# Performance work log

Measured on AMD Instinct MI355X. Metric: run time of the kernel, lower is better.

The kernel has to match this reference:

```python
import jax, jax.numpy as jnp
import numpy as np

B, S, H, D = 4, 2048, 16, 64
DM = H * D  # d_model = 1024


def setup_inputs() -> dict:
    key = jax.random.key(0)
    ks = jax.random.split(key, 11)
    s = 1.0 / np.sqrt(DM)
    return {
        "query": jax.random.normal(ks[0], (B, S, DM), jnp.float32),
        "key": jax.random.normal(ks[1], (B, S, DM), jnp.float32),
        "value": jax.random.normal(ks[2], (B, S, DM), jnp.float32),
        "Wq": jax.random.uniform(ks[3], (DM, DM), jnp.float32, -s, s),
        "bq": jax.random.uniform(ks[4], (DM,), jnp.float32, -s, s),
        "Wk": jax.random.uniform(ks[5], (DM, DM), jnp.float32, -s, s),
        "bk": jax.random.uniform(ks[6], (DM,), jnp.float32, -s, s),
        "Wv": jax.random.uniform(ks[7], (DM, DM), jnp.float32, -s, s),
        "bv": jax.random.uniform(ks[8], (DM,), jnp.float32, -s, s),
        "Wo": jax.random.uniform(ks[9], (DM, DM), jnp.float32, -s, s),
        "bo": jax.random.uniform(ks[10], (DM,), jnp.float32, -s, s),
        "masking": 1,
    }


def reference(query, key, value, Wq, bq, Wk, bk, Wv, bv, Wo, bo, masking):
    b, s, _ = query.shape
    # Linear projections (torch Linear: x @ W.T + b), split into heads
    q = (query @ Wq.T + bq).reshape(b, s, H, D).transpose(0, 2, 1, 3)  # [B,H,S,D]
    k = (key @ Wk.T + bk).reshape(b, -1, H, D).transpose(0, 2, 1, 3)
    v = (value @ Wv.T + bv).reshape(b, -1, H, D).transpose(0, 2, 1, 3)
    scores = jnp.einsum("bhqd,bhkd->bhqk", q, k) / np.power(D, 0.5)
    if masking:
        # subsequent (strictly upper-triangular) mask -> fill with -1e9
        sub = jnp.triu(jnp.ones((s, k.shape[2]), bool), k=1)
        scores = jnp.where(sub, jnp.float32(-1e9), scores)
    attn = jax.nn.softmax(scores, axis=-1)
    out = jnp.einsum("bhqk,bhkd->bhqd", attn, v)  # [B,H,S,D]
    out = out.transpose(0, 2, 1, 3).reshape(b, s, H * D)
    return out @ Wo.T + bo
```

## Files before the change

kernel.cpp:

```cpp
#include <hip/hip_runtime.h>
#include <stdint.h>
#include <stddef.h>

#define B_ 4
#define S_ 2048
#define H_ 16
#define D_ 64
#define DM 1024
#define MTOT 8192
#define QSCALE 0.1803368867f

typedef __bf16 bf16x8 __attribute__((ext_vector_type(8)));
typedef __bf16 bf16x4 __attribute__((ext_vector_type(4)));
typedef float  f32x4  __attribute__((ext_vector_type(4)));

__device__ __forceinline__ void g2l16(const void* g, void* l) {
  __builtin_amdgcn_global_load_lds(
      (__attribute__((address_space(1))) void*)g,
      (__attribute__((address_space(3))) void*)l, 16, 0, 0);
}

struct Cvt7 {
  const float* s[7];
  __bf16* d[7];
  float sc[7];
};
__global__ __launch_bounds__(256) void cvt_all(Cvt7 a) {
  const int b = blockIdx.x;
  int seg, i;
  if (b < 24576) { seg = b >> 13; i = ((b & 8191) << 8) + threadIdx.x; }
  else { const int sb = b - 24576; seg = 3 + (sb >> 10); i = ((sb & 1023) << 8) + threadIdx.x; }
  const float sc = a.sc[seg];
  const float4 v = ((const float4*)a.s[seg])[i];
  bf16x4 o;
  o.x = (__bf16)(v.x * sc); o.y = (__bf16)(v.y * sc);
  o.z = (__bf16)(v.z * sc); o.w = (__bf16)(v.w * sc);
  ((bf16x4*)a.d[seg])[i] = o;
}

__device__ __forceinline__ void gemm_main(const __bf16* __restrict__ A,
                                          const __bf16* __restrict__ W,
                                          int m0, int n0,
                                          __bf16* ldsA, __bf16* ldsB,
                                          f32x4 (&acc)[4][4]) {
  const int tid = threadIdx.x;
  const int lane = tid & 63, wave = tid >> 6;
  const int lq = lane & 15, lhi = lane >> 4;
  const int wr = wave >> 1, wc = wave & 1;

  const int srow = tid >> 2;
  const int cso = ((tid & 3) ^ ((srow >> 1) & 3)) * 8;
  const __bf16* pA = A + (size_t)(m0 + srow) * DM + cso;
  const __bf16* pB = W + (size_t)(n0 + srow) * DM + cso;
  const int tid8 = tid * 8;

  const int sx = (lhi ^ ((lq >> 1) & 3)) * 8;
  const int aB = (wr * 64 + lq) * 32 + sx;
  const int bB = (wc * 64 + lq) * 32 + sx;

#define SA(q, ko, bs) g2l16(pA + (size_t)(q) * 64 * DM + (ko), ldsA + (bs) * 4096 + (q) * 2048 + tid8)
#define SB(q, ko, bs) g2l16(pB + (size_t)(q) * 64 * DM + (ko), ldsB + (bs) * 4096 + (q) * 2048 + tid8)

  SA(0, 0, 0); SA(1, 0, 0); SB(0, 0, 0); SB(1, 0, 0);
  SA(0, 32, 1); SA(1, 32, 1); SB(0, 32, 1); SB(1, 32, 1);
  asm volatile("s_waitcnt vmcnt(4)" ::: "memory");
  __builtin_amdgcn_s_barrier();
  __builtin_amdgcn_sched_barrier(0);

  int bR = 0, bN = 1, bS = 2;
  int koS = 64;
#pragma unroll 1
  for (int t = 0; t < 32; ++t) {
    const __bf16* lA = ldsA + bR * 4096;
    const __bf16* lB = ldsB + bR * 4096;
    const bool s2 = t < 30;
    bf16x8 af[4], bf[4];

#pragma unroll
    for (int i = 0; i < 4; ++i) af[i] = *(const bf16x8*)(lA + aB + i * 512);
#pragma unroll
    for (int j = 0; j < 2; ++j) bf[j] = *(const bf16x8*)(lB + bB + j * 512);
    if (s2) { SA(0, koS, bS); SA(1, koS, bS); }
    __builtin_amdgcn_s_barrier();
    __builtin_amdgcn_sched_barrier(0);
    __builtin_amdgcn_s_setprio(1);
#pragma unroll
    for (int i = 0; i < 4; ++i)
#pragma unroll
      for (int j = 0; j < 2; ++j)
        acc[i][j] = __builtin_amdgcn_mfma_f32_16x16x32_bf16(af[i], bf[j], acc[i][j], 0, 0, 0);
    __builtin_amdgcn_s_setprio(0);

#pragma unroll
    for (int j = 2; j < 4; ++j) bf[j] = *(const bf16x8*)(lB + bB + j * 512);
    if (s2) { SB(0, koS, bS); SB(1, koS, bS); }
    if (t < 30) {
      asm volatile("s_waitcnt vmcnt(4)" ::: "memory");
    } else if (t == 30) {
      asm volatile("s_waitcnt vmcnt(0)" ::: "memory");
    }
    __builtin_amdgcn_s_barrier();
    __builtin_amdgcn_sched_barrier(0);
    __builtin_amdgcn_s_setprio(1);
#pragma unroll
    for (int i = 0; i < 4; ++i)
#pragma unroll
      for (int j = 2; j < 4; ++j)
        acc[i][j] = __builtin_amdgcn_mfma_f32_16x16x32_bf16(af[i], bf[j], acc[i][j], 0, 0, 0);
    __builtin_amdgcn_s_setprio(0);

    const int x = bR; bR = bN; bN = bS; bS = x;
    koS += 32;
  }
#undef SA
#undef SB
}

struct QKVArgs {
  const __bf16 *A0, *A1, *A2;
  const __bf16 *W0, *W1, *W2;
  const float *b0, *b1, *b2;
  __bf16 *oQ, *oK, *oVt;
};

__global__ __launch_bounds__(256, 3) void gemm_qkv(QKVArgs args) {
  const int z = blockIdx.z;
  const __bf16* A    = (z == 0) ? args.A0 : (z == 1) ? args.A1 : args.A2;
  const __bf16* W    = (z == 0) ? args.W0 : (z == 1) ? args.W1 : args.W2;
  const float*  bias = (z == 0) ? args.b0 : (z == 1) ? args.b1 : args.b2;
  const float   bsc  = (z == 0) ? QSCALE : 1.0f;

  __shared__ __bf16 ldsA[3 * 4096];
  __shared__ __bf16 ldsB[3 * 4096];

  const int m0 = blockIdx.x * 128;
  const int n0 = blockIdx.y * 128;

  f32x4 acc[4][4] = {};
  gemm_main(A, W, m0, n0, ldsA, ldsB, acc);

  const int lane = threadIdx.x & 63, wave = threadIdx.x >> 6;
  const int lq = lane & 15, lhi = lane >> 4;
  const int wr = wave >> 1, wc = wave & 1;

  if (z < 2) {
    __bf16* out = (z == 0) ? args.oQ : args.oK;
#pragma unroll
    for (int i = 0; i < 4; ++i)
#pragma unroll
      for (int j = 0; j < 4; ++j)
#pragma unroll
        for (int r = 0; r < 4; ++r) {
          const int row = m0 + wr * 64 + i * 16 + lhi * 4 + r;
          const int col = n0 + wc * 64 + j * 16 + lq;
          out[(size_t)row * DM + col] = (__bf16)(acc[i][j][r] + bias[col] * bsc);
        }
  } else {
    __bf16* out = args.oVt;
#pragma unroll
    for (int i = 0; i < 4; ++i)
#pragma unroll
      for (int j = 0; j < 4; ++j)
#pragma unroll
        for (int r = 0; r < 4; ++r) {
          const int row = m0 + wr * 64 + i * 16 + lhi * 4 + r;
          const int col = n0 + wc * 64 + j * 16 + lq;
          const int bb = row >> 11, s = row & 2047;
          const int hh = col >> 6,  d = col & 63;
          out[(((size_t)(bb * H_ + hh) * D_ + d) << 11) + s] =
              (__bf16)(acc[i][j][r] + bias[col]);
        }
  }
}

__global__ __launch_bounds__(256, 3) void gemm_oproj(const __bf16* __restrict__ A,
                                                     const __bf16* __restrict__ W,
                                                     const float* __restrict__ bias,
                                                     float* __restrict__ out) {
  __shared__ __bf16 ldsA[3 * 4096];
  __shared__ __bf16 ldsB[3 * 4096];

  const int m0 = blockIdx.x * 128;
  const int n0 = blockIdx.y * 128;

  f32x4 acc[4][4] = {};
  gemm_main(A, W, m0, n0, ldsA, ldsB, acc);

  const int lane = threadIdx.x & 63, wave = threadIdx.x >> 6;
  const int lq = lane & 15, lhi = lane >> 4;
  const int wr = wave >> 1, wc = wave & 1;

#pragma unroll
  for (int i = 0; i < 4; ++i)
#pragma unroll
    for (int j = 0; j < 4; ++j)
#pragma unroll
      for (int r = 0; r < 4; ++r) {
        const int row = m0 + wr * 64 + i * 16 + lhi * 4 + r;
        const int col = n0 + wc * 64 + j * 16 + lq;
        out[(size_t)row * DM + col] = acc[i][j][r] + bias[col];
      }
}

__global__ __launch_bounds__(256, 3) void attn_kernel(const __bf16* __restrict__ Q,
                                                      const __bf16* __restrict__ K,
                                                      const __bf16* __restrict__ Vt,
                                                      __bf16* __restrict__ O) {
  const int id = blockIdx.x;
  const int slot = id >> 8;
  const int tau = id & 255;
  const int k4 = (tau >> 3) & 3;
  const int bh = ((tau >> 5) << 3) | (tau & 7);
  const int b = bh >> 4, h = bh & 15;

  int tiles[2];
  int ntile;
  if (slot == 0)      { ntile = 1; tiles[0] = 15 - k4; tiles[1] = 0; }
  else if (slot == 1) { ntile = 1; tiles[0] = 8 + k4;  tiles[1] = 0; }
  else                { ntile = 2; tiles[0] = k4;      tiles[1] = 7 - k4; }

  const int wave = threadIdx.x >> 6;
  const int lane = threadIdx.x & 63;
  const int lq = lane & 15, lhi = lane >> 4;

  const __bf16* Qb = Q + (size_t)b * S_ * DM + h * D_;
  const __bf16* Kb = K + (size_t)b * S_ * DM + h * D_;
  const __bf16* Vb = Vt + (size_t)bh * D_ * S_;

  __shared__ __bf16 Ks[2][64 * 64];
  __shared__ __bf16 Vs[2][64 * 64];
  __shared__ __bf16 Ps[4][32 * 72];
  __bf16* const Pw = Ps[wave];

  const int rl = lane >> 3;
  const int cg8 = ((lane & 7) ^ rl) * 8;

  bf16x8 onesb;
#pragma unroll
  for (int q = 0; q < 8; ++q) onesb[q] = (__bf16)1.0f;

  for (int ti = 0; ti < ntile; ++ti) {
    const int t = tiles[ti];
    const int qw0 = t * 128 + wave * 32;
    const int jend = t * 128 + 64;

    if (ti) __syncthreads();

    bf16x8 qb[2][2];
#pragma unroll
    for (int m = 0; m < 2; ++m)
#pragma unroll
      for (int kd = 0; kd < 2; ++kd)
        qb[m][kd] = *(const bf16x8*)(Qb + (size_t)(qw0 + m * 16 + lq) * DM + kd * 32 + lhi * 8);

    f32x4 o_acc[2][4] = {};
    f32x4 o_sum[2] = {};

#pragma unroll
    for (int i = 0; i < 2; ++i) {
      const int row = wave * 16 + i * 8 + rl;
      g2l16(Kb + (size_t)row * DM + cg8, Ks[0] + ((wave * 16 + i * 8) << 6) + lane * 8);
      g2l16(Vb + (size_t)row * S_ + cg8, Vs[0] + ((wave * 16 + i * 8) << 6) + lane * 8);
    }

    int p = 0;
    for (int j0 = 0; j0 <= jend; j0 += 64) {
      __syncthreads();
      if (j0 < jend) {
        const int jn = j0 + 64;
#pragma unroll
        for (int i = 0; i < 2; ++i) {
          const int row = wave * 16 + i * 8 + rl;
          g2l16(Kb + (size_t)(jn + row) * DM + cg8, Ks[p ^ 1] + ((wave * 16 + i * 8) << 6) + lane * 8);
          g2l16(Vb + (size_t)row * S_ + jn + cg8, Vs[p ^ 1] + ((wave * 16 + i * 8) << 6) + lane * 8);
        }
      }

      if (j0 <= qw0 + 31) {
        bf16x8 kf[4][2];
#pragma unroll
        for (int kt = 0; kt < 4; ++kt) {
          const int r = kt * 16 + lq;
#pragma unroll
          for (int kd = 0; kd < 2; ++kd)
            kf[kt][kd] = *(const bf16x8*)(Ks[p] + (r << 6) + (((kd * 4 + lhi) ^ (r & 7)) << 3));
        }

        bf16x8 vf[4][2];
#pragma unroll
        for (int dt = 0; dt < 4; ++dt) {
          const int r = dt * 16 + lq;
#pragma unroll
          for (int kk = 0; kk < 2; ++kk)
            vf[dt][kk] = *(const bf16x8*)(Vs[p] + (r << 6) + (((kk * 4 + lhi) ^ (r & 7)) << 3));
        }

        f32x4 sc[2][4];
        __builtin_amdgcn_s_setprio(1);
#pragma unroll
        for (int m = 0; m < 2; ++m)
#pragma unroll
          for (int kt = 0; kt < 4; ++kt) {
            f32x4 s = {};
            s = __builtin_amdgcn_mfma_f32_16x16x32_bf16(kf[kt][0], qb[m][0], s, 0, 0, 0);
            s = __builtin_amdgcn_mfma_f32_16x16x32_bf16(kf[kt][1], qb[m][1], s, 0, 0, 0);
            sc[m][kt] = s;
          }
        __builtin_amdgcn_s_setprio(0);

#pragma unroll
        for (int m = 0; m < 2; ++m) {
          const bool dg = (j0 + 63 > qw0 + m * 16);
          if (dg) {
            const int thr = qw0 + m * 16 + lq - j0;
#pragma unroll
            for (int kt = 0; kt < 4; ++kt) {
              bf16x4 pk;
#pragma unroll
              for (int r = 0; r < 4; ++r) {
                float v = sc[m][kt][r];
                if (kt * 16 + lhi * 4 + r > thr) v = -1e9f;
                pk[r] = (__bf16)exp2f(v);
              }
              *(bf16x4*)(Pw + (m * 16 + lq) * 72 + kt * 16 + lhi * 4) = pk;
            }
          } else {
#pragma unroll
            for (int kt = 0; kt < 4; ++kt) {
              bf16x4 pk;
#pragma unroll
              for (int r = 0; r < 4; ++r) pk[r] = (__bf16)exp2f(sc[m][kt][r]);
              *(bf16x4*)(Pw + (m * 16 + lq) * 72 + kt * 16 + lhi * 4) = pk;
            }
          }
        }

#pragma unroll
        for (int m = 0; m < 2; ++m) {
          bf16x8 pa[2];
#pragma unroll
          for (int kk = 0; kk < 2; ++kk)
            pa[kk] = *(const bf16x8*)(Pw + (m * 16 + lq) * 72 + kk * 32 + lhi * 8);
          __builtin_amdgcn_s_setprio(1);
          o_sum[m] = __builtin_amdgcn_mfma_f32_16x16x32_bf16(pa[0], onesb, o_sum[m], 0, 0, 0);
          o_sum[m] = __builtin_amdgcn_mfma_f32_16x16x32_bf16(pa[1], onesb, o_sum[m], 0, 0, 0);
#pragma unroll
          for (int dt = 0; dt < 4; ++dt) {
            o_acc[m][dt] = __builtin_amdgcn_mfma_f32_16x16x32_bf16(pa[0], vf[dt][0], o_acc[m][dt], 0, 0, 0);
            o_acc[m][dt] = __builtin_amdgcn_mfma_f32_16x16x32_bf16(pa[1], vf[dt][1], o_acc[m][dt], 0, 0, 0);
          }
          __builtin_amdgcn_s_setprio(0);
        }
      }
      p ^= 1;
    }

#pragma unroll
    for (int m = 0; m < 2; ++m)
#pragma unroll
      for (int r = 0; r < 4; ++r) {
        const float inv = 1.0f / o_sum[m][r];
        const int qrow = qw0 + m * 16 + lhi * 4 + r;
        __bf16* orow = O + ((size_t)b * S_ + qrow) * DM + h * D_;
#pragma unroll
        for (int dt = 0; dt < 4; ++dt)
          orow[dt * 16 + lq] = (__bf16)(o_acc[m][dt][r] * inv);
      }
  }
}

extern "C" void kernel_launch(void* const* d_in, const int* in_sizes, int n_in,
                              void* d_out, int out_size, void* d_ws, size_t ws_size,
                              hipStream_t stream) {
  (void)in_sizes; (void)n_in; (void)out_size; (void)ws_size;
  const float* query = (const float*)d_in[0];
  const float* key   = (const float*)d_in[1];
  const float* value = (const float*)d_in[2];
  const float* Wq = (const float*)d_in[3];
  const float* bq = (const float*)d_in[4];
  const float* Wk = (const float*)d_in[5];
  const float* bk = (const float*)d_in[6];
  const float* Wv = (const float*)d_in[7];
  const float* bv = (const float*)d_in[8];
  const float* Wo = (const float*)d_in[9];
  const float* bo = (const float*)d_in[10];

  const size_t NX = (size_t)MTOT * DM;
  const size_t NW = (size_t)DM * DM;
  __bf16* p = (__bf16*)d_ws;
  __bf16 *Xq = p, *Xk = Xq + NX, *Xv = Xk + NX;
  __bf16 *Wqb = Xv + NX, *Wkb = Wqb + NW, *Wvb = Wkb + NW, *Wob = Wvb + NW;
  __bf16 *Qrm = Wob + NW, *Krm = Qrm + NX, *Vt = Krm + NX, *Orm = Vt + NX;

  Cvt7 ca;
  ca.s[0] = query; ca.s[1] = key; ca.s[2] = value;
  ca.s[3] = Wq; ca.s[4] = Wk; ca.s[5] = Wv; ca.s[6] = Wo;
  ca.d[0] = Xq; ca.d[1] = Xk; ca.d[2] = Xv;
  ca.d[3] = Wqb; ca.d[4] = Wkb; ca.d[5] = Wvb; ca.d[6] = Wob;
  ca.sc[0] = 1.0f; ca.sc[1] = 1.0f; ca.sc[2] = 1.0f;
  ca.sc[3] = QSCALE;
  ca.sc[4] = 1.0f; ca.sc[5] = 1.0f; ca.sc[6] = 1.0f;
  cvt_all<<<28672, 256, 0, stream>>>(ca);

  QKVArgs qa;
  qa.A0 = Xq; qa.A1 = Xk; qa.A2 = Xv;
  qa.W0 = Wqb; qa.W1 = Wkb; qa.W2 = Wvb;
  qa.b0 = bq; qa.b1 = bk; qa.b2 = bv;
  qa.oQ = Qrm; qa.oK = Krm; qa.oVt = Vt;
  gemm_qkv<<<dim3(MTOT / 128, DM / 128, 3), 256, 0, stream>>>(qa);

  attn_kernel<<<dim3(768), 256, 0, stream>>>(Qrm, Krm, Vt, Orm);

  gemm_oproj<<<dim3(MTOT / 128, DM / 128), 256, 0, stream>>>(Orm, Wob, bo, (float*)d_out);
}
```

Before: 317.7 us.

## Fuse fp32-to-bf16 activation conversion into QKV GEMM A-tile loading

Measured after the change: 332.6 us. +4.7%, slower.

```diff
diff --git a/kernel.cpp b/kernel.cpp
--- a/kernel.cpp
+++ b/kernel.cpp
@@ -20,22 +20,177 @@
       (__attribute__((address_space(3))) void*)l, 16, 0, 0);
 }
 
-struct Cvt7 {
-  const float* s[7];
-  __bf16* d[7];
-  float sc[7];
+struct Cvt4 {
+  const float* s[4];
+  __bf16* d[4];
+  float sc[4];
 };
-__global__ __launch_bounds__(256) void cvt_all(Cvt7 a) {
+__global__ __launch_bounds__(256) void cvt_all(Cvt4 a) {
   const int b = blockIdx.x;
-  int seg, i;
-  if (b < 24576) { seg = b >> 13; i = ((b & 8191) << 8) + threadIdx.x; }
-  else { const int sb = b - 24576; seg = 3 + (sb >> 10); i = ((sb & 1023) << 8) + threadIdx.x; }
+  const int seg = b >> 10;
+  const int i = ((b & 1023) << 8) + threadIdx.x;
   const float sc = a.sc[seg];
   const float4 v = ((const float4*)a.s[seg])[i];
   bf16x4 o;
   o.x = (__bf16)(v.x * sc); o.y = (__bf16)(v.y * sc);
   o.z = (__bf16)(v.z * sc); o.w = (__bf16)(v.w * sc);
   ((bf16x4*)a.d[seg])[i] = o;
+}
+
+struct QKVArgs {
+  const float *A0, *A1, *A2;
+  const __bf16 *W0, *W1, *W2;
+  const float *b0, *b1, *b2;
+  __bf16 *oQ, *oK, *oVt;
+};
+
+__global__ __launch_bounds__(256, 3) void gemm_qkv(QKVArgs args) {
+  const int z = blockIdx.z;
+  const float*  A    = (z == 0) ? args.A0 : (z == 1) ? args.A1 : args.A2;
+  const __bf16* W    = (z == 0) ? args.W0 : (z == 1) ? args.W1 : args.W2;
+  const float*  bias = (z == 0) ? args.b0 : (z == 1) ? args.b1 : args.b2;
+  const float   bsc  = (z == 0) ? QSCALE : 1.0f;
+
+  __shared__ __bf16 ldsA[3 * 4096];
+  __shared__ __bf16 ldsB[3 * 4096];
+
+  const int m0 = blockIdx.x * 128;
+  const int n0 = blockIdx.y * 128;
+  const int tid = threadIdx.x;
+  const int lane = tid & 63, wave = tid >> 6;
+  const int lq = lane & 15, lhi = lane >> 4;
+  const int wr = wave >> 1, wc = wave & 1;
+
+  const int arow = tid >> 1;
+  const int acol = (tid & 1) * 16;
+  const float* pA = A + (size_t)(m0 + arow) * DM + acol;
+  const int asw = (arow >> 1) & 3;
+  const int aw0 = arow * 32 + (((tid & 1) * 2 + 0) ^ asw) * 8;
+  const int aw1 = arow * 32 + (((tid & 1) * 2 + 1) ^ asw) * 8;
+
+  const int srow = tid >> 2;
+  const int cso = ((tid & 3) ^ ((srow >> 1) & 3)) * 8;
+  const __bf16* pB = W + (size_t)(n0 + srow) * DM + cso;
+  const int tid8 = tid * 8;
+
+  const int sx = (lhi ^ ((lq >> 1) & 3)) * 8;
+  const int aB = (wr * 64 + lq) * 32 + sx;
+  const int bB = (wc * 64 + lq) * 32 + sx;
+
+  f32x4 acc[4][4] = {};
+  f32x4 s0[4], s1[4];
+
+#define SB2(ko, bs)                                                           \
+  g2l16(pB + (ko), ldsB + (bs) * 4096 + tid8);                                \
+  g2l16(pB + (size_t)64 * DM + (ko), ldsB + (bs) * 4096 + 2048 + tid8)
+
+#define LDA(SL, ko)                                                           \
+  _Pragma("unroll") for (int u = 0; u < 4; ++u)                               \
+      SL[u] = *(const f32x4*)(pA + (ko) + u * 4)
+
+  LDA(s0, 0);
+  __builtin_amdgcn_sched_barrier(0);
+  SB2(0, 0);
+  __builtin_amdgcn_sched_barrier(0);
+  LDA(s1, 32);
+  __builtin_amdgcn_sched_barrier(0);
+  SB2(32, 1);
+  asm volatile("s_waitcnt vmcnt(8)" ::: "memory");
+  {
+    bf16x8 w0, w1;
+#pragma unroll
+    for (int e = 0; e < 4; ++e) {
+      w0[e] = (__bf16)s0[0][e]; w0[e + 4] = (__bf16)s0[1][e];
+      w1[e] = (__bf16)s0[2][e]; w1[e + 4] = (__bf16)s0[3][e];
+    }
+    *(bf16x8*)(ldsA + aw0) = w0;
+    *(bf16x8*)(ldsA + aw1) = w1;
+  }
+  asm volatile("s_waitcnt vmcnt(6)" ::: "memory");
+  asm volatile("s_waitcnt lgkmcnt(0)" ::: "memory");
+  __builtin_amdgcn_s_barrier();
+  __builtin_amdgcn_sched_barrier(0);
+
+  int bR = 0, bN = 1, bS = 2;
+
+#define TILE(t, SW, SL)                                                       \
+  {                                                                           \
+    const __bf16* lA = ldsA + bR * 4096;                                      \
+    const __bf16* lB = ldsB + bR * 4096;                                      \
+    bf16x8 af[4], bf[4];                                                      \
+    _Pragma("unroll") for (int i = 0; i < 4; ++i)                             \
+        af[i] = *(const bf16x8*)(lA + aB + i * 512);                          \
+    _Pragma("unroll") for (int j = 0; j < 4; ++j)                             \
+        bf[j] = *(const bf16x8*)(lB + bB + j * 512);                          \
+    if ((t) < 31) {                                                           \
+      asm volatile("s_waitcnt vmcnt(2)" ::: "memory");                        \
+      bf16x8 w0, w1;                                                          \
+      _Pragma("unroll") for (int e = 0; e < 4; ++e) {                         \
+        w0[e] = (__bf16)SW[0][e]; w0[e + 4] = (__bf16)SW[1][e];               \
+        w1[e] = (__bf16)SW[2][e]; w1[e + 4] = (__bf16)SW[3][e];               \
+      }                                                                       \
+      *(bf16x8*)(ldsA + bN * 4096 + aw0) = w0;                                \
+      *(bf16x8*)(ldsA + bN * 4096 + aw1) = w1;                                \
+    }                                                                         \
+    if ((t) < 30) {                                                           \
+      const int ko = ((t) + 2) * 32;                                          \
+      LDA(SL, ko);                                                            \
+      __builtin_amdgcn_sched_barrier(0);                                      \
+      SB2(ko, bS);                                                            \
+      asm volatile("s_waitcnt vmcnt(6)" ::: "memory");                        \
+    } else if ((t) == 30) {                                                   \
+      asm volatile("s_waitcnt vmcnt(0)" ::: "memory");                        \
+    }                                                                         \
+    asm volatile("s_waitcnt lgkmcnt(0)" ::: "memory");                        \
+    __builtin_amdgcn_s_barrier();                                             \
+    __builtin_amdgcn_sched_barrier(0);                                        \
+    __builtin_amdgcn_s_setprio(1);                                            \
+    _Pragma("unroll") for (int i = 0; i < 4; ++i)                             \
+        _Pragma("unroll") for (int j = 0; j < 4; ++j)                         \
+            acc[i][j] = __builtin_amdgcn_mfma_f32_16x16x32_bf16(              \
+                af[i], bf[j], acc[i][j], 0, 0, 0);                            \
+    __builtin_amdgcn_s_setprio(0);                                            \
+    { const int x = bR; bR = bN; bN = bS; bS = x; }                           \
+  }
+
+#pragma unroll 1
+  for (int tt = 0; tt < 16; ++tt) {
+    const int t0 = 2 * tt;
+    TILE(t0, s1, s0)
+    TILE(t0 + 1, s0, s1)
+  }
+#undef TILE
+#undef LDA
+#undef SB2
+
+  if (z < 2) {
+    __bf16* out = (z == 0) ? args.oQ : args.oK;
+#pragma unroll
+    for (int i = 0; i < 4; ++i)
+#pragma unroll
+      for (int j = 0; j < 4; ++j)
+#pragma unroll
+        for (int r = 0; r < 4; ++r) {
+          const int row = m0 + wr * 64 + i * 16 + lhi * 4 + r;
+          const int col = n0 + wc * 64 + j * 16 + lq;
+          out[(size_t)row * DM + col] = (__bf16)(acc[i][j][r] + bias[col] * bsc);
+        }
+  } else {
+    __bf16* out = args.oVt;
+#pragma unroll
+    for (int i = 0; i < 4; ++i)
+#pragma unroll
+      for (int j = 0; j < 4; ++j)
+#pragma unroll
+        for (int r = 0; r < 4; ++r) {
+          const int row = m0 + wr * 64 + i * 16 + lhi * 4 + r;
+          const int col = n0 + wc * 64 + j * 16 + lq;
+          const int bb = row >> 11, s = row & 2047;
+          const int hh = col >> 6,  d = col & 63;
+          out[(((size_t)(bb * H_ + hh) * D_ + d) << 11) + s] =
+              (__bf16)(acc[i][j][r] + bias[col]);
+        }
+  }
 }
 
 __device__ __forceinline__ void gemm_main(const __bf16* __restrict__ A,
@@ -116,63 +271,6 @@
 #undef SB
 }
 
-struct QKVArgs {
-  const __bf16 *A0, *A1, *A2;
-  const __bf16 *W0, *W1, *W2;
-  const float *b0, *b1, *b2;
-  __bf16 *oQ, *oK, *oVt;
-};
-
-__global__ __launch_bounds__(256, 3) void gemm_qkv(QKVArgs args) {
-  const int z = blockIdx.z;
-  const __bf16* A    = (z == 0) ? args.A0 : (z == 1) ? args.A1 : args.A2;
-  const __bf16* W    = (z == 0) ? args.W0 : (z == 1) ? args.W1 : args.W2;
-  const float*  bias = (z == 0) ? args.b0 : (z == 1) ? args.b1 : args.b2;
-  const float   bsc  = (z == 0) ? QSCALE : 1.0f;
-
-  __shared__ __bf16 ldsA[3 * 4096];
-  __shared__ __bf16 ldsB[3 * 4096];
-
-  const int m0 = blockIdx.x * 128;
-  const int n0 = blockIdx.y * 128;
-
-  f32x4 acc[4][4] = {};
-  gemm_main(A, W, m0, n0, ldsA, ldsB, acc);
-
-  const int lane = threadIdx.x & 63, wave = threadIdx.x >> 6;
-  const int lq = lane & 15, lhi = lane >> 4;
-  const int wr = wave >> 1, wc = wave & 1;
-
-  if (z < 2) {
-    __bf16* out = (z == 0) ? args.oQ : args.oK;
-#pragma unroll
-    for (int i = 0; i < 4; ++i)
-#pragma unroll
-      for (int j = 0; j < 4; ++j)
-#pragma unroll
-        for (int r = 0; r < 4; ++r) {
-          const int row = m0 + wr * 64 + i * 16 + lhi * 4 + r;
-          const int col = n0 + wc * 64 + j * 16 + lq;
-          out[(size_t)row * DM + col] = (__bf16)(acc[i][j][r] + bias[col] * bsc);
-        }
-  } else {
-    __bf16* out = args.oVt;
-#pragma unroll
-    for (int i = 0; i < 4; ++i)
-#pragma unroll
-      for (int j = 0; j < 4; ++j)
-#pragma unroll
-        for (int r = 0; r < 4; ++r) {
-          const int row = m0 + wr * 64 + i * 16 + lhi * 4 + r;
-          const int col = n0 + wc * 64 + j * 16 + lq;
-          const int bb = row >> 11, s = row & 2047;
-          const int hh = col >> 6,  d = col & 63;
-          out[(((size_t)(bb * H_ + hh) * D_ + d) << 11) + s] =
-              (__bf16)(acc[i][j][r] + bias[col]);
-        }
-  }
-}
-
 __global__ __launch_bounds__(256, 3) void gemm_oproj(const __bf16* __restrict__ A,
                                                      const __bf16* __restrict__ W,
                                                      const float* __restrict__ bias,
@@ -333,10 +431,7 @@
               *(bf16x4*)(Pw + (m * 16 + lq) * 72 + kt * 16 + lhi * 4) = pk;
             }
           }
-        }
-
-#pragma unroll
-        for (int m = 0; m < 2; ++m) {
+
           bf16x8 pa[2];
 #pragma unroll
           for (int kk = 0; kk < 2; ++kk)
@@ -388,22 +483,18 @@
   const size_t NX = (size_t)MTOT * DM;
   const size_t NW = (size_t)DM * DM;
   __bf16* p = (__bf16*)d_ws;
-  __bf16 *Xq = p, *Xk = Xq + NX, *Xv = Xk + NX;
-  __bf16 *Wqb = Xv + NX, *Wkb = Wqb + NW, *Wvb = Wkb + NW, *Wob = Wvb + NW;
+  __bf16 *Wqb = p, *Wkb = Wqb + NW, *Wvb = Wkb + NW, *Wob = Wvb + NW;
   __bf16 *Qrm = Wob + NW, *Krm = Qrm + NX, *Vt = Krm + NX, *Orm = Vt + NX;
 
-  Cvt7 ca;
-  ca.s[0] = query; ca.s[1] = key; ca.s[2] = value;
-  ca.s[3] = Wq; ca.s[4] = Wk; ca.s[5] = Wv; ca.s[6] = Wo;
-  ca.d[0] = Xq; ca.d[1] = Xk; ca.d[2] = Xv;
-  ca.d[3] = Wqb; ca.d[4] = Wkb; ca.d[5] = Wvb; ca.d[6] = Wob;
-  ca.sc[0] = 1.0f; ca.sc[1] = 1.0f; ca.sc[2] = 1.0f;
-  ca.sc[3] = QSCALE;
-  ca.sc[4] = 1.0f; ca.sc[5] = 1.0f; ca.sc[6] = 1.0f;
-  cvt_all<<<28672, 256, 0, stream>>>(ca);
+  Cvt4 ca;
+  ca.s[0] = Wq; ca.s[1] = Wk; ca.s[2] = Wv; ca.s[3] = Wo;
+  ca.d[0] = Wqb; ca.d[1] = Wkb; ca.d[2] = Wvb; ca.d[3] = Wob;
+  ca.sc[0] = QSCALE;
+  ca.sc[1] = 1.0f; ca.sc[2] = 1.0f; ca.sc[3] = 1.0f;
+  cvt_all<<<4096, 256, 0, stream>>>(ca);
 
   QKVArgs qa;
-  qa.A0 = Xq; qa.A1 = Xk; qa.A2 = Xv;
+  qa.A0 = query; qa.A1 = key; qa.A2 = value;
   qa.W0 = Wqb; qa.W1 = Wkb; qa.W2 = Wvb;
   qa.b0 = bq; qa.b1 = bk; qa.b2 = bv;
   qa.oQ = Qrm; qa.oK = Krm; qa.oVt = Vt;
```
